# Performance work log

Measured on AMD Instinct MI355X. Metric: run time of the kernel, lower is better.

Reference implementation:

```python
import jax, jax.numpy as jnp
import numpy as np

DIM = 1024
HEADS = 16
HEAD_DIM = DIM // HEADS
HIDDEN = 4 * DIM
EPS = 1e-5


def _layernorm(x, g, b):
    mu = jnp.mean(x, axis=-1, keepdims=True)
    var = jnp.mean(jnp.square(x - mu), axis=-1, keepdims=True)
    return (x - mu) * jax.lax.rsqrt(var + EPS) * g + b


def setup_inputs() -> dict:
    key = jax.random.key(0)
    ks = jax.random.split(key, 8)
    s = lambda fan_in: 1.0 / np.sqrt(fan_in)
    return {
        "x": jax.random.normal(ks[0], (8, 1024, DIM), dtype=jnp.float32),
        "ln1_g": jnp.ones((DIM,), jnp.float32),
        "ln1_b": jnp.zeros((DIM,), jnp.float32),
        "w_qkv": jax.random.normal(ks[1], (3 * DIM, DIM), jnp.float32) * s(DIM),
        "w_proj": jax.random.normal(ks[2], (DIM, DIM), jnp.float32) * s(DIM),
        "b_proj": jnp.zeros((DIM,), jnp.float32),
        "ln2_g": jnp.ones((DIM,), jnp.float32),
        "ln2_b": jnp.zeros((DIM,), jnp.float32),
        "w_fc1": jax.random.normal(ks[3], (HIDDEN, DIM), jnp.float32) * s(DIM),
        "b_fc1": jnp.zeros((HIDDEN,), jnp.float32),
        "w_fc2": jax.random.normal(ks[4], (DIM, HIDDEN), jnp.float32) * s(HIDDEN),
        "b_fc2": jnp.zeros((DIM,), jnp.float32),
    }


def reference(x, ln1_g, ln1_b, w_qkv, w_proj, b_proj, ln2_g, ln2_b, w_fc1, b_fc1, w_fc2, b_fc2):
    B, N, C = x.shape
    # --- attention branch (pre-norm) ---
    xn = _layernorm(x, ln1_g, ln1_b)
    qkv = xn @ w_qkv.T  # [B,N,3C]
    qkv = qkv.reshape(B, N, 3, HEADS, HEAD_DIM)
    q = qkv[:, :, 0].transpose(0, 2, 1, 3)  # [B,H,N,D]
    k = qkv[:, :, 1].transpose(0, 2, 1, 3)
    v = qkv[:, :, 2].transpose(0, 2, 1, 3)
    scale = HEAD_DIM ** -0.5
    scores = jnp.einsum("bhqd,bhkd->bhqk", q, k) * scale
    attn = jax.nn.softmax(scores, axis=-1)  # [B,H,N,N]
    y = jnp.einsum("bhqk,bhkd->bhqd", attn, v)
    y = y.transpose(0, 2, 1, 3).reshape(B, N, C)
    y = y @ w_proj.T + b_proj
    x = x + y
    # --- MLP branch (pre-norm) ---
    xn2 = _layernorm(x, ln2_g, ln2_b)
    h = jax.nn.gelu(xn2 @ w_fc1.T + b_fc1, approximate=False)
    x = x + (h @ w_fc2.T + b_fc2)
    return (x, attn)
```

## Files before the change

### kernel.cpp

```cpp
#include <hip/hip_runtime.h>
#include <cstdint>
#include <math.h>


typedef _Float16 f16;
typedef _Float16 f16x4 __attribute__((ext_vector_type(4)));
typedef _Float16 f16x8 __attribute__((ext_vector_type(8)));
typedef float f32x4 __attribute__((ext_vector_type(4)));

#define DEV static __device__ __forceinline__

DEV void gload16(const void* g, void* l) {
  __builtin_amdgcn_global_load_lds(
      (__attribute__((address_space(1))) void*)(uintptr_t)g,
      (__attribute__((address_space(3))) void*)(uintptr_t)l, 16, 0, 0);
}

DEV f32x4 mfma16(f16x8 a, f16x8 b, f32x4 c) {
  return __builtin_amdgcn_mfma_f32_16x16x32_f16(a, b, c, 0, 0, 0);
}

DEV void nt_core64(const f16* __restrict__ A, const f16* __restrict__ B,
                   size_t lda, size_t ldb, int K, f16* As, f16* Bs,
                   f32x4 acc[4][4])
{
  const int tid  = threadIdx.x;
  const int lane = tid & 63;
  const int w    = tid >> 6;
  const int wm   = (w >> 1) << 6;
  const int wn   = (w & 1) << 6;
  const int frow = lane & 15;
  const int lg   = lane >> 4;

  const int srow0 = w * 32 + (lane >> 3);
  const int scol  = ((lane & 7) ^ ((lane >> 3) & 7)) << 3;
  const f16* Ab = A + (size_t)srow0 * lda + scol;
  const f16* Bb = B + (size_t)srow0 * ldb + scol;
  f16* la = As + w * 2048 + lane * 8;
  f16* lb = Bs + w * 2048 + lane * 8;

  for (int k0 = 0; k0 < K; k0 += 64) {
#pragma unroll
    for (int L = 0; L < 4; ++L)
      gload16(Ab + (size_t)(L * 8) * lda + k0, la + L * 512);
#pragma unroll
    for (int L = 0; L < 4; ++L)
      gload16(Bb + (size_t)(L * 8) * ldb + k0, lb + L * 512);
    __syncthreads();
#pragma unroll
    for (int kc = 0; kc < 2; ++kc) {
      f16x8 af[4], bf[4];
#pragma unroll
      for (int i = 0; i < 4; ++i) {
        const int ra = wm + i * 16 + frow;
        const int rb = wn + i * 16 + frow;
        af[i] = *(const f16x8*)(As + ra * 64 + ((((kc << 2) + lg) ^ (ra & 7)) << 3));
        bf[i] = *(const f16x8*)(Bs + rb * 64 + ((((kc << 2) + lg) ^ (rb & 7)) << 3));
      }
#pragma unroll
      for (int i = 0; i < 4; ++i)
#pragma unroll
        for (int j = 0; j < 4; ++j)
          acc[i][j] = mfma16(af[i], bf[j], acc[i][j]);
    }
    __syncthreads();
  }
}

__global__ __launch_bounds__(256) void k_cvtall(const float* __restrict__ s0,
                                                const float* __restrict__ s1,
                                                const float* __restrict__ s2,
                                                const float* __restrict__ s3,
                                                f16* __restrict__ out)
{
  const int i = blockIdx.x * blockDim.x + threadIdx.x;
  const float* src;
  int off;
  if (i < 786432)       { src = s0; off = 0; }
  else if (i < 1048576) { src = s1; off = 786432; }
  else if (i < 2097152) { src = s2; off = 1048576; }
  else                  { src = s3; off = 2097152; }
  const float4 f = ((const float4*)src)[i - off];
  f16x4 o; o[0] = (f16)f.x; o[1] = (f16)f.y; o[2] = (f16)f.z; o[3] = (f16)f.w;
  ((f16x4*)out)[i] = o;
}

__global__ __launch_bounds__(256) void k_ln(const float* __restrict__ xin,
                                            const float* __restrict__ g,
                                            const float* __restrict__ bb,
                                            f16* __restrict__ out)
{
  __shared__ float red[8];
  const int tid = threadIdx.x;
  const size_t row = blockIdx.x;
  const float4 v = ((const float4*)(xin + row * 1024))[tid];
  float s  = v.x + v.y + v.z + v.w;
  float sq = v.x * v.x + v.y * v.y + v.z * v.z + v.w * v.w;
#pragma unroll
  for (int off = 32; off > 0; off >>= 1) { s += __shfl_xor(s, off); sq += __shfl_xor(sq, off); }
  if ((tid & 63) == 0) { red[tid >> 6] = s; red[4 + (tid >> 6)] = sq; }
  __syncthreads();
  s  = red[0] + red[1] + red[2] + red[3];
  sq = red[4] + red[5] + red[6] + red[7];
  const float mu = s * (1.0f / 1024.0f);
  const float rs = rsqrtf(sq * (1.0f / 1024.0f) - mu * mu + 1e-5f);
  const float4 gg = ((const float4*)g)[tid];
  const float4 bv = ((const float4*)bb)[tid];
  f16x4 o;
  o[0] = (f16)((v.x - mu) * rs * gg.x + bv.x);
  o[1] = (f16)((v.y - mu) * rs * gg.y + bv.y);
  o[2] = (f16)((v.z - mu) * rs * gg.z + bv.z);
  o[3] = (f16)((v.w - mu) * rs * gg.w + bv.w);
  ((f16x4*)(out + row * 1024))[tid] = o;
}

__global__ __launch_bounds__(256) void k_qkv(const f16* __restrict__ xn,
                                             const f16* __restrict__ wq,
                                             f16* __restrict__ qb, f16* __restrict__ kb,
                                             f16* __restrict__ vT)
{
  __shared__ __align__(16) f16 As[8192], Bs[8192];
  f32x4 acc[4][4] = {};
  const int bm = blockIdx.x, bn = blockIdx.y;
  nt_core64(xn + (size_t)bm * 128 * 1024, wq + (size_t)bn * 128 * 1024,
            1024, 1024, 1024, As, Bs, acc);
  const int tid = threadIdx.x, lane = tid & 63, w = tid >> 6;
  const int r0 = bm * 128 + ((w >> 1) << 6) + ((lane >> 4) << 2);
  const int c0 = bn * 128 + ((w & 1) << 6);
  const int sec = (bn * 128) >> 10;
#pragma unroll
  for (int i = 0; i < 4; ++i) {
#pragma unroll
    for (int j = 0; j < 4; ++j) {
      const int o = c0 + j * 16 + (lane & 15);
      const int h = (o & 1023) >> 6, d = o & 63;
#pragma unroll
      for (int e = 0; e < 4; ++e) {
        const int m = r0 + i * 16 + e;
        const int b = m >> 10, n = m & 1023;
        const int bh = (b << 4) + h;
        const f16 val = (f16)acc[i][j][e];
        if (sec == 0)      qb[((size_t)bh * 1024 + n) * 64 + d] = val;
        else if (sec == 1) kb[((size_t)bh * 1024 + n) * 64 + d] = val;
        else               vT[((size_t)bh * 64 + d) * 1024 + n] = val;
      }
    }
  }
}

__global__ __launch_bounds__(256) void k_attn(const f16* __restrict__ qb,
                                              const f16* __restrict__ kb,
                                              const f16* __restrict__ vT,
                                              float* __restrict__ attn,
                                              f16* __restrict__ y2)
{
  __shared__ __align__(16) f16 P[32 * 1024];
  const int tid = threadIdx.x, lane = tid & 63, w = tid >> 6;
  const int lr = lane & 15, lg = lane >> 4;
  const int bh = blockIdx.y;
  const int m0 = blockIdx.x * 32;
  const f16* Qb = qb + ((size_t)bh << 16);
  const f16* Kb = kb + ((size_t)bh << 16);
  const f16* Vt = vT + ((size_t)bh << 16);

  f16x8 qf[2][2];
#pragma unroll
  for (int i = 0; i < 2; ++i)
#pragma unroll
    for (int ks = 0; ks < 2; ++ks)
      qf[i][ks] = *(const f16x8*)(Qb + (size_t)(m0 + i * 16 + lr) * 64 + ks * 32 + lg * 8);

  for (int cc = 0; cc < 4; ++cc) {
    const int cb = (w << 8) + (cc << 6);
    f16x8 bf[4][2];
#pragma unroll
    for (int j = 0; j < 4; ++j)
#pragma unroll
      for (int ks = 0; ks < 2; ++ks)
        bf[j][ks] = *(const f16x8*)(Kb + (size_t)(cb + j * 16 + lr) * 64 + ks * 32 + lg * 8);
    f32x4 acc[2][4] = {};
#pragma unroll
    for (int i = 0; i < 2; ++i)
#pragma unroll
      for (int j = 0; j < 4; ++j) {
        acc[i][j] = mfma16(qf[i][0], bf[j][0], acc[i][j]);
        acc[i][j] = mfma16(qf[i][1], bf[j][1], acc[i][j]);
      }
#pragma unroll
    for (int i = 0; i < 2; ++i)
#pragma unroll
      for (int j = 0; j < 4; ++j)
#pragma unroll
        for (int e = 0; e < 4; ++e) {
          const int r = i * 16 + (lg << 2) + e;
          const int c = cb + j * 16 + lr;
          P[(r << 10) + (((c >> 3) ^ (r & 7)) << 3) + (c & 7)] = (f16)(acc[i][j][e] * 0.125f);
        }
  }
  __syncthreads();

  const int r2 = tid >> 3;
  f16* Prow = P + (r2 << 10);
  const int rx = r2 & 7;
  f16x8 vv[16];
  float mrow = -1e30f;
#pragma unroll
  for (int q = 0; q < 16; ++q) {
    const int c = (tid & 7) + (q << 3);
    vv[q] = *(const f16x8*)(Prow + ((c ^ rx) << 3));
#pragma unroll
    for (int e = 0; e < 8; ++e) mrow = fmaxf(mrow, (float)vv[q][e]);
  }
  mrow = fmaxf(mrow, __shfl_xor(mrow, 1));
  mrow = fmaxf(mrow, __shfl_xor(mrow, 2));
  mrow = fmaxf(mrow, __shfl_xor(mrow, 4));
  float ssum = 0.f;
#pragma unroll
  for (int q = 0; q < 16; ++q) {
#pragma unroll
    for (int e = 0; e < 8; ++e) {
      const float ev = __expf((float)vv[q][e] - mrow);
      ssum += ev;
      vv[q][e] = (f16)ev;
    }
  }
  ssum += __shfl_xor(ssum, 1);
  ssum += __shfl_xor(ssum, 2);
  ssum += __shfl_xor(ssum, 4);
  const float inv = 1.0f / ssum;
  float* Aout = attn + ((size_t)bh << 20) + ((size_t)(m0 + r2) << 10);
#pragma unroll
  for (int q = 0; q < 16; ++q) {
    const int c = (tid & 7) + (q << 3);
    f16x8 nv;
    f32x4 o0, o1;
    o0[0] = (float)vv[q][0] * inv; o0[1] = (float)vv[q][1] * inv;
    o0[2] = (float)vv[q][2] * inv; o0[3] = (float)vv[q][3] * inv;
    o1[0] = (float)vv[q][4] * inv; o1[1] = (float)vv[q][5] * inv;
    o1[2] = (float)vv[q][6] * inv; o1[3] = (float)vv[q][7] * inv;
#pragma unroll
    for (int e = 0; e < 8; ++e) nv[e] = (f16)((float)vv[q][e] * inv);
    __builtin_nontemporal_store(o0, (f32x4*)(Aout + (c << 3)));
    __builtin_nontemporal_store(o1, (f32x4*)(Aout + (c << 3)) + 1);
    *(f16x8*)(Prow + ((c ^ rx) << 3)) = nv;
  }
  __syncthreads();

  const int dc = w << 4;
  f32x4 acc2[2] = {};
#pragma unroll 4
  for (int k0 = 0; k0 < 1024; k0 += 32) {
    const f16x8 bf = *(const f16x8*)(Vt + (size_t)(dc + lr) * 1024 + k0 + lg * 8);
#pragma unroll
    for (int i = 0; i < 2; ++i) {
      const int ra = i * 16 + lr;
      const int ch = (k0 >> 3) + lg;
      const f16x8 af = *(const f16x8*)(P + (ra << 10) + ((ch ^ (ra & 7)) << 3));
      acc2[i] = mfma16(af, bf, acc2[i]);
    }
  }
  const int b = bh >> 4, h = bh & 15;
#pragma unroll
  for (int i = 0; i < 2; ++i)
#pragma unroll
    for (int e = 0; e < 4; ++e) {
      const int rloc = i * 16 + (lg << 2) + e;
      y2[(size_t)(b * 1024 + m0 + rloc) * 1024 + (h << 6) + dc + lr] = (f16)acc2[i][e];
    }
}

__global__ __launch_bounds__(256) void k_proj(const f16* __restrict__ y2,
                                              const f16* __restrict__ wp,
                                              const float* __restrict__ bproj,
                                              const float* __restrict__ x,
                                              float* __restrict__ xmid)
{
  __shared__ __align__(16) f16 As[8192], Bs[8192];
  f32x4 acc[4][4] = {};
  nt_core64(y2 + (size_t)blockIdx.x * 128 * 1024, wp + (size_t)blockIdx.y * 128 * 1024,
            1024, 1024, 1024, As, Bs, acc);
  const int tid = threadIdx.x, lane = tid & 63, w = tid >> 6;
  const int r0 = blockIdx.x * 128 + ((w >> 1) << 6) + ((lane >> 4) << 2);
  const int c0 = blockIdx.y * 128 + ((w & 1) << 6) + (lane & 15);
#pragma unroll
  for (int i = 0; i < 4; ++i)
#pragma unroll
    for (int j = 0; j < 4; ++j) {
      const int c = c0 + j * 16;
      const float bias = bproj[c];
#pragma unroll
      for (int e = 0; e < 4; ++e) {
        const size_t idx = (size_t)(r0 + i * 16 + e) * 1024 + c;
        xmid[idx] = acc[i][j][e] + bias + x[idx];
      }
    }
}

__global__ __launch_bounds__(256) void k_fc1(const f16* __restrict__ xn,
                                             const f16* __restrict__ wf,
                                             const float* __restrict__ bfc1,
                                             f16* __restrict__ hb)
{
  __shared__ __align__(16) f16 As[8192], Bs[8192];
  f32x4 acc[4][4] = {};
  nt_core64(xn + (size_t)blockIdx.x * 128 * 1024, wf + (size_t)blockIdx.y * 128 * 1024,
            1024, 1024, 1024, As, Bs, acc);
  const int tid = threadIdx.x, lane = tid & 63, w = tid >> 6;
  const int r0 = blockIdx.x * 128 + ((w >> 1) << 6) + ((lane >> 4) << 2);
  const int c0 = blockIdx.y * 128 + ((w & 1) << 6) + (lane & 15);
#pragma unroll
  for (int i = 0; i < 4; ++i)
#pragma unroll
    for (int j = 0; j < 4; ++j) {
      const int c = c0 + j * 16;
      const float bias = bfc1[c];
#pragma unroll
      for (int e = 0; e < 4; ++e) {
        const float t = acc[i][j][e] + bias;
        const float ge = 0.5f * t * (1.0f + erff(t * 0.70710678118654752f));
        hb[(size_t)(r0 + i * 16 + e) * 4096 + c] = (f16)ge;
      }
    }
}

__global__ __launch_bounds__(256) void k_fc2(const f16* __restrict__ hb,
                                             const f16* __restrict__ wf,
                                             const float* __restrict__ bfc2,
                                             const float* __restrict__ xmid,
                                             float* __restrict__ out)
{
  __shared__ __align__(16) f16 As[8192], Bs[8192];
  f32x4 acc[4][4] = {};
  nt_core64(hb + (size_t)blockIdx.x * 128 * 4096, wf + (size_t)blockIdx.y * 128 * 4096,
            4096, 4096, 4096, As, Bs, acc);
  const int tid = threadIdx.x, lane = tid & 63, w = tid >> 6;
  const int r0 = blockIdx.x * 128 + ((w >> 1) << 6) + ((lane >> 4) << 2);
  const int c0 = blockIdx.y * 128 + ((w & 1) << 6) + (lane & 15);
#pragma unroll
  for (int i = 0; i < 4; ++i)
#pragma unroll
    for (int j = 0; j < 4; ++j) {
      const int c = c0 + j * 16;
      const float bias = bfc2[c];
#pragma unroll
      for (int e = 0; e < 4; ++e) {
        const size_t idx = (size_t)(r0 + i * 16 + e) * 1024 + c;
        out[idx] = acc[i][j][e] + bias + xmid[idx];
      }
    }
}

extern "C" void kernel_launch(void* const* d_in, const int* in_sizes, int n_in,
                              void* d_out, int out_size, void* d_ws, size_t ws_size,
                              hipStream_t stream)
{
  const float* x     = (const float*)d_in[0];
  const float* ln1g  = (const float*)d_in[1];
  const float* ln1b  = (const float*)d_in[2];
  const float* wqkv  = (const float*)d_in[3];
  const float* wproj = (const float*)d_in[4];
  const float* bproj = (const float*)d_in[5];
  const float* ln2g  = (const float*)d_in[6];
  const float* ln2b  = (const float*)d_in[7];
  const float* wfc1  = (const float*)d_in[8];
  const float* bfc1  = (const float*)d_in[9];
  const float* wfc2  = (const float*)d_in[10];
  const float* bfc2  = (const float*)d_in[11];

  char* ws = (char*)d_ws;
  f16* wqkv_h  = (f16*)(ws);
  f16* wproj_h = (f16*)(ws + 6291456);
  f16* wfc1_h  = (f16*)(ws + 8388608);
  f16* wfc2_h  = (f16*)(ws + 16777216);
  f16* xn      = (f16*)(ws + 25165824);
  f16* qb      = (f16*)(ws + 41943040);
  f16* kb      = (f16*)(ws + 58720256);
  f16* vT      = (f16*)(ws + 75497472);
  f16* y2      = (f16*)(ws + 92274688);
  float* xmid  = (float*)(ws + 109051904);
  f16* hb      = (f16*)(ws + 41943040);

  float* out_x = (float*)d_out;
  float* attn  = (float*)d_out + 8388608;

  k_cvtall<<<12288, 256, 0, stream>>>(wqkv, wproj, wfc1, wfc2, wqkv_h);
  k_ln<<<8192, 256, 0, stream>>>(x, ln1g, ln1b, xn);
  k_qkv<<<dim3(64, 24), 256, 0, stream>>>(xn, wqkv_h, qb, kb, vT);
  k_attn<<<dim3(32, 128), 256, 0, stream>>>(qb, kb, vT, attn, y2);
  k_proj<<<dim3(64, 8), 256, 0, stream>>>(y2, wproj_h, bproj, x, xmid);
  k_ln<<<8192, 256, 0, stream>>>(xmid, ln2g, ln2b, xn);
  k_fc1<<<dim3(64, 32), 256, 0, stream>>>(xn, wfc1_h, bfc1, hb);
  k_fc2<<<dim3(64, 8), 256, 0, stream>>>(hb, wfc2_h, bfc2, xmid, out_x);
}
```

Baseline: 524.0 us.

## Merge weight conversion with first layernorm, remap attention blocks, cheaper GELU

Folds the fp32-to-fp16 weight conversion and the first layernorm into one launch, saving a kernel launch and letting the two independent jobs overlap. Remaps attention block indices so consecutive workgroups are spread across heads, which may change cache or XCD locality. Swaps erff in the FC1 epilogue for an Abramowitz-Stegun polynomial erf approximation using __expf, which is cheaper but less accurate.

```diff
diff --git a/kernel.cpp b/kernel.cpp
--- a/kernel.cpp
+++ b/kernel.cpp
@@ -18,6 +18,16 @@
 
 DEV f32x4 mfma16(f16x8 a, f16x8 b, f32x4 c) {
   return __builtin_amdgcn_mfma_f32_16x16x32_f16(a, b, c, 0, 0, 0);
+}
+
+DEV float gelu_f(float v) {
+  const float a = fabsf(v) * 0.70710678118654752f;
+  const float t = 1.0f / (1.0f + 0.3275911f * a);
+  const float p = t * (0.254829592f + t * (-0.284496736f + t * (1.421413741f +
+                  t * (-1.453152027f + t * 1.061405429f))));
+  const float e = p * __expf(-a * a);
+  const float erfv = v >= 0.f ? (1.f - e) : (e - 1.f);
+  return 0.5f * v * (1.0f + erfv);
 }
 
 DEV void nt_core64(const f16* __restrict__ A, const f16* __restrict__ B,
@@ -67,22 +77,51 @@
   }
 }
 
-__global__ __launch_bounds__(256) void k_cvtall(const float* __restrict__ s0,
+__global__ __launch_bounds__(256) void k_cvt_ln(const float* __restrict__ s0,
                                                 const float* __restrict__ s1,
                                                 const float* __restrict__ s2,
                                                 const float* __restrict__ s3,
-                                                f16* __restrict__ out)
-{
-  const int i = blockIdx.x * blockDim.x + threadIdx.x;
-  const float* src;
-  int off;
-  if (i < 786432)       { src = s0; off = 0; }
-  else if (i < 1048576) { src = s1; off = 786432; }
-  else if (i < 2097152) { src = s2; off = 1048576; }
-  else                  { src = s3; off = 2097152; }
-  const float4 f = ((const float4*)src)[i - off];
-  f16x4 o; o[0] = (f16)f.x; o[1] = (f16)f.y; o[2] = (f16)f.z; o[3] = (f16)f.w;
-  ((f16x4*)out)[i] = o;
+                                                f16* __restrict__ wout,
+                                                const float* __restrict__ xin,
+                                                const float* __restrict__ g,
+                                                const float* __restrict__ bb,
+                                                f16* __restrict__ xnout)
+{
+  __shared__ float red[8];
+  const int tid = threadIdx.x;
+  if (blockIdx.x < 12288) {
+    const int i = blockIdx.x * 256 + tid;
+    const float* src;
+    int off;
+    if (i < 786432)       { src = s0; off = 0; }
+    else if (i < 1048576) { src = s1; off = 786432; }
+    else if (i < 2097152) { src = s2; off = 1048576; }
+    else                  { src = s3; off = 2097152; }
+    const float4 f = ((const float4*)src)[i - off];
+    f16x4 o; o[0] = (f16)f.x; o[1] = (f16)f.y; o[2] = (f16)f.z; o[3] = (f16)f.w;
+    ((f16x4*)wout)[i] = o;
+    return;
+  }
+  const size_t row = blockIdx.x - 12288;
+  const float4 v = ((const float4*)(xin + row * 1024))[tid];
+  float s  = v.x + v.y + v.z + v.w;
+  float sq = v.x * v.x + v.y * v.y + v.z * v.z + v.w * v.w;
+#pragma unroll
+  for (int off = 32; off > 0; off >>= 1) { s += __shfl_xor(s, off); sq += __shfl_xor(sq, off); }
+  if ((tid & 63) == 0) { red[tid >> 6] = s; red[4 + (tid >> 6)] = sq; }
+  __syncthreads();
+  s  = red[0] + red[1] + red[2] + red[3];
+  sq = red[4] + red[5] + red[6] + red[7];
+  const float mu = s * (1.0f / 1024.0f);
+  const float rs = rsqrtf(sq * (1.0f / 1024.0f) - mu * mu + 1e-5f);
+  const float4 gg = ((const float4*)g)[tid];
+  const float4 bv = ((const float4*)bb)[tid];
+  f16x4 o;
+  o[0] = (f16)((v.x - mu) * rs * gg.x + bv.x);
+  o[1] = (f16)((v.y - mu) * rs * gg.y + bv.y);
+  o[2] = (f16)((v.z - mu) * rs * gg.z + bv.z);
+  o[3] = (f16)((v.w - mu) * rs * gg.w + bv.w);
+  ((f16x4*)(xnout + row * 1024))[tid] = o;
 }
 
 __global__ __launch_bounds__(256) void k_ln(const float* __restrict__ xin,
@@ -157,8 +196,10 @@
   __shared__ __align__(16) f16 P[32 * 1024];
   const int tid = threadIdx.x, lane = tid & 63, w = tid >> 6;
   const int lr = lane & 15, lg = lane >> 4;
-  const int bh = blockIdx.y;
-  const int m0 = blockIdx.x * 32;
+  const int flat = blockIdx.y * 32 + blockIdx.x;
+  const int id2 = (flat & 7) * 512 + (flat >> 3);
+  const int bh = id2 >> 5;
+  const int m0 = (id2 & 31) * 32;
   const f16* Qb = qb + ((size_t)bh << 16);
   const f16* Kb = kb + ((size_t)bh << 16);
   const f16* Vt = vT + ((size_t)bh << 16);
@@ -317,8 +358,7 @@
 #pragma unroll
       for (int e = 0; e < 4; ++e) {
         const float t = acc[i][j][e] + bias;
-        const float ge = 0.5f * t * (1.0f + erff(t * 0.70710678118654752f));
-        hb[(size_t)(r0 + i * 16 + e) * 4096 + c] = (f16)ge;
+        hb[(size_t)(r0 + i * 16 + e) * 4096 + c] = (f16)gelu_f(t);
       }
     }
 }
@@ -383,8 +423,8 @@
   float* out_x = (float*)d_out;
   float* attn  = (float*)d_out + 8388608;
 
-  k_cvtall<<<12288, 256, 0, stream>>>(wqkv, wproj, wfc1, wfc2, wqkv_h);
-  k_ln<<<8192, 256, 0, stream>>>(x, ln1g, ln1b, xn);
+  k_cvt_ln<<<12288 + 8192, 256, 0, stream>>>(wqkv, wproj, wfc1, wfc2, wqkv_h,
+                                             x, ln1g, ln1b, xn);
   k_qkv<<<dim3(64, 24), 256, 0, stream>>>(xn, wqkv_h, qb, kb, vT);
   k_attn<<<dim3(32, 128), 256, 0, stream>>>(qb, kb, vT, attn, y2);
   k_proj<<<dim3(64, 8), 256, 0, stream>>>(y2, wproj_h, bproj, x, xmid);
```

Result: faster. 502.0 us (-4.2%).
